# Optimization experiments

Measured on AMD Instinct MI355X. Metric: run time of the kernel, lower is better.

## Reference

```python
import jax, jax.numpy as jnp
import numpy as np

N_NODES = 100000
N_EDGES = 1600000
DIMS = [64, 64, 64, 32]  # [n_feat] + hid


def setup_inputs() -> dict:
    key = jax.random.key(0)
    ks = jax.random.split(key, 2 + 2 * (len(DIMS) - 1))
    x = jax.random.normal(ks[0], (N_NODES, DIMS[0]), dtype=jnp.float32)
    edge_index = jax.random.randint(ks[1], (2, N_EDGES), 0, N_NODES, dtype=jnp.int64)
    inp = {"x": x, "edge_index": edge_index}
    for i in range(len(DIMS) - 1):
        fan_in, fan_out = DIMS[i], DIMS[i + 1]
        scale = 1.0 / np.sqrt(fan_in)
        inp[f"W{i+1}"] = jax.random.normal(ks[2 + 2 * i], (fan_in, fan_out), dtype=jnp.float32) * scale
        inp[f"b{i+1}"] = jax.random.normal(ks[3 + 2 * i], (fan_out,), dtype=jnp.float32) * scale
    return inp


def _gcn_conv(x, W, b, src, dst, dis):
    # h = X W ; out[i] = sum_{j->i} norm_ij * h[j] + dis[i]^2 * h[i] + b
    h = x @ W
    norm = dis[src] * dis[dst]                      # [E]
    agg = jax.ops.segment_sum(h[src] * norm[:, None], dst, num_segments=x.shape[0])
    agg = agg + h * (dis * dis)[:, None]            # self-loop contribution
    return agg + b


def reference(x, edge_index, W1, b1, W2, b2, W3, b3):
    src, dst = edge_index[0], edge_index[1]
    n = x.shape[0]
    # degree with self-loops (edge weight 1), symmetric normalization
    deg = jax.ops.segment_sum(jnp.ones(src.shape[0], x.dtype), dst, num_segments=n) + 1.0
    dis = jax.lax.rsqrt(deg)
    h = jax.nn.relu(_gcn_conv(x, W1, b1, src, dst, dis))   # dropout is identity in eval
    h = jax.nn.relu(_gcn_conv(h, W2, b2, src, dst, dis))
    return _gcn_conv(h, W3, b3, src, dst, dis)
```

## Files before the change

### kernel.cpp

```cpp
#include <hip/hip_runtime.h>


typedef __attribute__((ext_vector_type(8))) _Float16 half8;

static inline int cdiv(int a, int b) { return (a + b - 1) / b; }

#define ACHUNK 8192
#define MAXNBK 512

__global__ void k_bucket_hist(const int* __restrict__ dst, int* __restrict__ counts_t,
                              int NBK, int NBA, int E) {
    __shared__ int cnt[MAXNBK];
    int t = threadIdx.x, b = blockIdx.x;
    for (int i = t; i < NBK; i += 256) cnt[i] = 0;
    __syncthreads();
    int e0 = b * ACHUNK;
#pragma unroll 8
    for (int j = 0; j < ACHUNK / 256; ++j) {
        int e = e0 + j * 256 + t;
        if (e < E) atomicAdd(&cnt[dst[e] >> 8], 1);
    }
    __syncthreads();
    for (int i = t; i < NBK; i += 256) counts_t[i * NBA + b] = cnt[i];
}

#define SCAN_T 256
#define SCAN_V 4
#define SCAN_CHUNK 1024

__global__ void k_scan_partial(const int* __restrict__ a, int* __restrict__ bsum, int n) {
    __shared__ int red[SCAN_T];
    int t = threadIdx.x, b = blockIdx.x;
    int base = b * SCAN_CHUNK + t * SCAN_V;
    int s = 0;
#pragma unroll
    for (int j = 0; j < SCAN_V; ++j) { int i = base + j; if (i < n) s += a[i]; }
    red[t] = s;
    __syncthreads();
    for (int off = SCAN_T / 2; off > 0; off >>= 1) {
        if (t < off) red[t] += red[t + off];
        __syncthreads();
    }
    if (t == 0) bsum[b] = red[0];
}

__global__ void k_scan_final(const int* __restrict__ a, const int* __restrict__ bsum,
                             int* __restrict__ out, int nb, int n) {
    __shared__ int sb[256];
    __shared__ int sh[SCAN_T];
    int t = threadIdx.x, bk = blockIdx.x;
    sb[t] = (t < nb) ? bsum[t] : 0;
    __syncthreads();
    for (int off = 1; off < 256; off <<= 1) {
        int u = (t >= off) ? sb[t - off] : 0;
        __syncthreads();
        sb[t] += u;
        __syncthreads();
    }
    int bbase = (bk == 0) ? 0 : sb[bk - 1];
    int base = bk * SCAN_CHUNK + t * SCAN_V;
    int v[SCAN_V];
    int s = 0;
#pragma unroll
    for (int j = 0; j < SCAN_V; ++j) {
        int i = base + j;
        v[j] = (i < n) ? a[i] : 0;
        s += v[j];
    }
    sh[t] = s;
    __syncthreads();
    for (int off = 1; off < SCAN_T; off <<= 1) {
        int u = (t >= off) ? sh[t - off] : 0;
        __syncthreads();
        sh[t] += u;
        __syncthreads();
    }
    int run = sh[t] - s + bbase;
#pragma unroll
    for (int j = 0; j < SCAN_V; ++j) {
        int i = base + j;
        if (i < n) { out[i] = run; run += v[j]; }
    }
}

__global__ void k_bucket_scatter(const int* __restrict__ src, const int* __restrict__ dst,
                                 const int* __restrict__ offsets, unsigned* __restrict__ bucketed,
                                 int NBK, int NBA, int E) {
    __shared__ int curs[MAXNBK];
    int t = threadIdx.x, b = blockIdx.x;
    for (int i = t; i < NBK; i += 256) curs[i] = offsets[i * NBA + b];
    __syncthreads();
    int e0 = b * ACHUNK;
#pragma unroll 8
    for (int j = 0; j < ACHUNK / 256; ++j) {
        int e = e0 + j * 256 + t;
        if (e < E) {
            int d = dst[e];
            int pos = atomicAdd(&curs[d >> 8], 1);
            bucketed[pos] = (unsigned)src[e] | ((unsigned)(d & 255) << 24);
        }
    }
}

__global__ void k_bucket_build(const unsigned* __restrict__ bucketed,
                               const int* __restrict__ offsets,
                               int* __restrict__ csr_src, int* __restrict__ row_start,
                               float* __restrict__ dis, int NBK, int NBA, int N, int E) {
    __shared__ int cnt[256];
    __shared__ int sc[256];
    int t = threadIdx.x, k = blockIdx.x;
    int base = offsets[k * NBA];
    int end = (k + 1 < NBK) ? offsets[(k + 1) * NBA] : E;
    cnt[t] = 0;
    __syncthreads();
    for (int i = base + t; i < end; i += 256)
        atomicAdd(&cnt[bucketed[i] >> 24], 1);
    __syncthreads();
    int c = cnt[t];
    sc[t] = c;
    __syncthreads();
    for (int off = 1; off < 256; off <<= 1) {
        int u = (t >= off) ? sc[t - off] : 0;
        __syncthreads();
        sc[t] += u;
        __syncthreads();
    }
    int excl = sc[t] - c;
    int node = k * 256 + t;
    if (node < N) {
        row_start[node] = base + excl;
        dis[node] = rsqrtf(1.0f + (float)c);
    }
    if (k == 0 && t == 0) row_start[N] = E;
    cnt[t] = base + excl;
    __syncthreads();
    for (int i = base + t; i < end; i += 256) {
        unsigned w = bucketed[i];
        int pos = atomicAdd(&cnt[w >> 24], 1);
        csr_src[pos] = (int)(w & 0xFFFFFFu);
    }
}

template <int K, int M>
__device__ inline void gemm_core(const float* Ws, const float* Xs,
                                 const float* __restrict__ dis,
                                 _Float16* __restrict__ H, int row0, int n) {
    constexpr int CPT = 8;
    constexpr int TPR = M / CPT;
    constexpr int KP = K + 1;
    int tid = threadIdx.x;
    int r = tid / TPR, c0 = (tid % TPR) * CPT;
    int row = row0 + r;
    if (row >= n) return;
    float4 a0 = make_float4(0.f, 0.f, 0.f, 0.f);
    float4 a1 = make_float4(0.f, 0.f, 0.f, 0.f);
#pragma unroll
    for (int k = 0; k < K; ++k) {
        float xv = Xs[r * KP + k];
        float4 w0 = ((const float4*)Ws)[(k * M + c0) / 4];
        float4 w1 = ((const float4*)Ws)[(k * M + c0) / 4 + 1];
        a0.x = fmaf(xv, w0.x, a0.x);
        a0.y = fmaf(xv, w0.y, a0.y);
        a0.z = fmaf(xv, w0.z, a0.z);
        a0.w = fmaf(xv, w0.w, a0.w);
        a1.x = fmaf(xv, w1.x, a1.x);
        a1.y = fmaf(xv, w1.y, a1.y);
        a1.z = fmaf(xv, w1.z, a1.z);
        a1.w = fmaf(xv, w1.w, a1.w);
    }
    float dn = dis[row];
    half8 hv;
    hv[0] = (_Float16)(a0.x * dn);
    hv[1] = (_Float16)(a0.y * dn);
    hv[2] = (_Float16)(a0.z * dn);
    hv[3] = (_Float16)(a0.w * dn);
    hv[4] = (_Float16)(a1.x * dn);
    hv[5] = (_Float16)(a1.y * dn);
    hv[6] = (_Float16)(a1.z * dn);
    hv[7] = (_Float16)(a1.w * dn);
    ((half8*)H)[(size_t)row * (M / CPT) + c0 / CPT] = hv;
}

template <int K, int M>
__global__ void k_gemm_f(const float* __restrict__ X, const float* __restrict__ W,
                         const float* __restrict__ dis, _Float16* __restrict__ H, int n) {
    constexpr int TPR = M / 8;
    constexpr int ROWS = 256 / TPR;
    constexpr int KP = K + 1;
    __shared__ float Ws[K * M];
    __shared__ float Xs[ROWS * KP];
    int tid = threadIdx.x;
    for (int idx = tid; idx < K * M / 4; idx += 256)
        ((float4*)Ws)[idx] = ((const float4*)W)[idx];
    int row0 = blockIdx.x * ROWS;
    for (int idx = tid; idx < ROWS * (K / 4); idx += 256) {
        int r = idx / (K / 4), kq = idx % (K / 4);
        int row = row0 + r;
        float4 vv = (row < n) ? ((const float4*)X)[(size_t)row * (K / 4) + kq]
                              : make_float4(0.f, 0.f, 0.f, 0.f);
        Xs[r * KP + kq * 4 + 0] = vv.x;
        Xs[r * KP + kq * 4 + 1] = vv.y;
        Xs[r * KP + kq * 4 + 2] = vv.z;
        Xs[r * KP + kq * 4 + 3] = vv.w;
    }
    __syncthreads();
    gemm_core<K, M>(Ws, Xs, dis, H, row0, n);
}

template <int K, int M>
__global__ void k_gemm_h(const _Float16* __restrict__ X, const float* __restrict__ W,
                         const float* __restrict__ dis, _Float16* __restrict__ H, int n) {
    constexpr int TPR = M / 8;
    constexpr int ROWS = 256 / TPR;
    constexpr int KP = K + 1;
    __shared__ float Ws[K * M];
    __shared__ float Xs[ROWS * KP];
    int tid = threadIdx.x;
    for (int idx = tid; idx < K * M / 4; idx += 256)
        ((float4*)Ws)[idx] = ((const float4*)W)[idx];
    int row0 = blockIdx.x * ROWS;
    for (int idx = tid; idx < ROWS * (K / 8); idx += 256) {
        int r = idx / (K / 8), kq = idx % (K / 8);
        int row = row0 + r;
        if (row < n) {
            half8 v = ((const half8*)X)[(size_t)row * (K / 8) + kq];
#pragma unroll
            for (int j = 0; j < 8; ++j) Xs[r * KP + kq * 8 + j] = (float)v[j];
        } else {
#pragma unroll
            for (int j = 0; j < 8; ++j) Xs[r * KP + kq * 8 + j] = 0.f;
        }
    }
    __syncthreads();
    gemm_core<K, M>(Ws, Xs, dis, H, row0, n);
}

__device__ inline void store8(float* out, int node, int fl, int LPN, const float* r) {
    float4* op = (float4*)(out + ((size_t)node * LPN + fl) * 8);
    op[0] = make_float4(r[0], r[1], r[2], r[3]);
    op[1] = make_float4(r[4], r[5], r[6], r[7]);
}
__device__ inline void store8(_Float16* out, int node, int fl, int LPN, const float* r) {
    half8 v;
#pragma unroll
    for (int j = 0; j < 8; ++j) v[j] = (_Float16)r[j];
    ((half8*)out)[(size_t)node * LPN + fl] = v;
}

template <int M, bool RELU, typename OutT>
__global__ void k_aggregate(const _Float16* __restrict__ h, const float* __restrict__ dis,
                            const int* __restrict__ row_start, const int* __restrict__ csr_src,
                            const float* __restrict__ b, OutT* __restrict__ out, int n) {
    constexpr int LPN = M / 8;
    constexpr int NPW = 64 / LPN;
    int gtid = blockIdx.x * blockDim.x + threadIdx.x;
    int wave = gtid >> 6;
    int lane = threadIdx.x & 63;
    int sub = lane / LPN, fl = lane % LPN;
    int node = wave * NPW + sub;
    if (node >= n) return;
    const half8* h8 = (const half8*)h;
    float acc[8];
#pragma unroll
    for (int j = 0; j < 8; ++j) acc[j] = 0.f;
    int e = row_start[node], e1 = row_start[node + 1];
    for (; e + 1 < e1; e += 2) {
        int s0 = csr_src[e];
        int s1 = csr_src[e + 1];
        half8 v0 = h8[(size_t)s0 * LPN + fl];
        half8 v1 = h8[(size_t)s1 * LPN + fl];
#pragma unroll
        for (int j = 0; j < 8; ++j) acc[j] += (float)v0[j] + (float)v1[j];
    }
    if (e < e1) {
        int s0 = csr_src[e];
        half8 v0 = h8[(size_t)s0 * LPN + fl];
#pragma unroll
        for (int j = 0; j < 8; ++j) acc[j] += (float)v0[j];
    }
    float dn = dis[node];
    half8 hv = h8[(size_t)node * LPN + fl];
    float4 b0 = ((const float4*)b)[fl * 2];
    float4 b1 = ((const float4*)b)[fl * 2 + 1];
    float r[8];
    r[0] = (acc[0] + (float)hv[0]) * dn + b0.x;
    r[1] = (acc[1] + (float)hv[1]) * dn + b0.y;
    r[2] = (acc[2] + (float)hv[2]) * dn + b0.z;
    r[3] = (acc[3] + (float)hv[3]) * dn + b0.w;
    r[4] = (acc[4] + (float)hv[4]) * dn + b1.x;
    r[5] = (acc[5] + (float)hv[5]) * dn + b1.y;
    r[6] = (acc[6] + (float)hv[6]) * dn + b1.z;
    r[7] = (acc[7] + (float)hv[7]) * dn + b1.w;
    if (RELU) {
#pragma unroll
        for (int j = 0; j < 8; ++j) r[j] = fmaxf(r[j], 0.f);
    }
    store8(out, node, fl, LPN, r);
}

extern "C" void kernel_launch(void* const* d_in, const int* in_sizes, int n_in,
                              void* d_out, int out_size, void* d_ws, size_t ws_size,
                              hipStream_t stream) {
    const float* x   = (const float*)d_in[0];
    const int*   ei  = (const int*)d_in[1];
    const float* W1  = (const float*)d_in[2];
    const float* b1  = (const float*)d_in[3];
    const float* W2  = (const float*)d_in[4];
    const float* b2  = (const float*)d_in[5];
    const float* W3  = (const float*)d_in[6];
    const float* b3  = (const float*)d_in[7];
    float* out = (float*)d_out;

    const int N = in_sizes[0] / 64;
    const int E = in_sizes[1] / 2;
    const int* src = ei;
    const int* dst = ei + E;

    const int NBK = cdiv(N, 256);
    const int NBA = cdiv(E, ACHUNK);
    const int nmat = NBK * NBA;

    const size_t Np = (size_t)((N + 63) / 64) * 64;
    char* p = (char*)d_ws;
    int*      counts_t = (int*)p;      p += (size_t)nmat * sizeof(int);
    int*      offsets  = (int*)p;      p += (size_t)nmat * sizeof(int);
    int*      bsum     = (int*)p;      p += 1024 * sizeof(int);
    int*      row_start= (int*)p;      p += (Np + 64) * sizeof(int);
    float*    dis      = (float*)p;    p += Np * sizeof(float);
    unsigned* bucketed = (unsigned*)p; p += (size_t)E * sizeof(unsigned);
    int*      csr_src  = (int*)p;      p += (size_t)E * sizeof(int);
    _Float16* bufH     = (_Float16*)p; p += Np * 64 * sizeof(_Float16);
    _Float16* bufX     = (_Float16*)p; p += Np * 64 * sizeof(_Float16);
    (void)ws_size;

    const int B = 256;
    const int nb = cdiv(nmat, SCAN_CHUNK);

    k_bucket_hist<<<NBA, B, 0, stream>>>(dst, counts_t, NBK, NBA, E);
    k_scan_partial<<<nb, B, 0, stream>>>(counts_t, bsum, nmat);
    k_scan_final<<<nb, B, 0, stream>>>(counts_t, bsum, offsets, nb, nmat);
    k_bucket_scatter<<<NBA, B, 0, stream>>>(src, dst, offsets, bucketed, NBK, NBA, E);
    k_bucket_build<<<NBK, B, 0, stream>>>(bucketed, offsets, csr_src, row_start, dis,
                                          NBK, NBA, N, E);

    const int blocks_a64 = cdiv(cdiv(N, 8) * 64, B);
    const int blocks_a32 = cdiv(cdiv(N, 16) * 64, B);

    k_gemm_f<64, 64><<<cdiv(N, 32), B, 0, stream>>>(x, W1, dis, bufH, N);
    k_aggregate<64, true, _Float16><<<blocks_a64, B, 0, stream>>>(
        bufH, dis, row_start, csr_src, b1, bufX, N);

    k_gemm_h<64, 64><<<cdiv(N, 32), B, 0, stream>>>(bufX, W2, dis, bufH, N);
    k_aggregate<64, true, _Float16><<<blocks_a64, B, 0, stream>>>(
        bufH, dis, row_start, csr_src, b2, bufX, N);

    k_gemm_h<64, 32><<<cdiv(N, 64), B, 0, stream>>>(bufX, W3, dis, bufH, N);
    k_aggregate<32, false, float><<<blocks_a32, B, 0, stream>>>(
        bufH, dis, row_start, csr_src, b3, out, N);
}
```

Before: 342.2 us.

## Fuse neighbor aggregation with next-layer GEMM and unroll edge loop by four

Replaces the separate aggregate and GEMM kernels for layers 1→2 and 2→3 with one kernel. Each block aggregates 32 nodes into shared memory, applies bias and ReLU, then multiplies by the next weight matrix. This removes the round trip of the intermediate fp16 activation through global memory and two kernel launches. The edge loop is also unrolled by four to keep more gathers in flight. In exchange, blocks are larger and use more shared memory. For the 32-wide output layer only half the threads do GEMM work.

```diff
diff --git a/kernel.cpp b/kernel.cpp
--- a/kernel.cpp
+++ b/kernel.cpp
@@ -139,46 +139,6 @@
         int pos = atomicAdd(&cnt[w >> 24], 1);
         csr_src[pos] = (int)(w & 0xFFFFFFu);
     }
-}
-
-template <int K, int M>
-__device__ inline void gemm_core(const float* Ws, const float* Xs,
-                                 const float* __restrict__ dis,
-                                 _Float16* __restrict__ H, int row0, int n) {
-    constexpr int CPT = 8;
-    constexpr int TPR = M / CPT;
-    constexpr int KP = K + 1;
-    int tid = threadIdx.x;
-    int r = tid / TPR, c0 = (tid % TPR) * CPT;
-    int row = row0 + r;
-    if (row >= n) return;
-    float4 a0 = make_float4(0.f, 0.f, 0.f, 0.f);
-    float4 a1 = make_float4(0.f, 0.f, 0.f, 0.f);
-#pragma unroll
-    for (int k = 0; k < K; ++k) {
-        float xv = Xs[r * KP + k];
-        float4 w0 = ((const float4*)Ws)[(k * M + c0) / 4];
-        float4 w1 = ((const float4*)Ws)[(k * M + c0) / 4 + 1];
-        a0.x = fmaf(xv, w0.x, a0.x);
-        a0.y = fmaf(xv, w0.y, a0.y);
-        a0.z = fmaf(xv, w0.z, a0.z);
-        a0.w = fmaf(xv, w0.w, a0.w);
-        a1.x = fmaf(xv, w1.x, a1.x);
-        a1.y = fmaf(xv, w1.y, a1.y);
-        a1.z = fmaf(xv, w1.z, a1.z);
-        a1.w = fmaf(xv, w1.w, a1.w);
-    }
-    float dn = dis[row];
-    half8 hv;
-    hv[0] = (_Float16)(a0.x * dn);
-    hv[1] = (_Float16)(a0.y * dn);
-    hv[2] = (_Float16)(a0.z * dn);
-    hv[3] = (_Float16)(a0.w * dn);
-    hv[4] = (_Float16)(a1.x * dn);
-    hv[5] = (_Float16)(a1.y * dn);
-    hv[6] = (_Float16)(a1.z * dn);
-    hv[7] = (_Float16)(a1.w * dn);
-    ((half8*)H)[(size_t)row * (M / CPT) + c0 / CPT] = hv;
 }
 
 template <int K, int M>
@@ -204,55 +164,131 @@
         Xs[r * KP + kq * 4 + 3] = vv.w;
     }
     __syncthreads();
-    gemm_core<K, M>(Ws, Xs, dis, H, row0, n);
-}
-
-template <int K, int M>
-__global__ void k_gemm_h(const _Float16* __restrict__ X, const float* __restrict__ W,
-                         const float* __restrict__ dis, _Float16* __restrict__ H, int n) {
-    constexpr int TPR = M / 8;
-    constexpr int ROWS = 256 / TPR;
-    constexpr int KP = K + 1;
-    __shared__ float Ws[K * M];
-    __shared__ float Xs[ROWS * KP];
+    int r = tid / TPR, c0 = (tid % TPR) * 8;
+    int row = row0 + r;
+    if (row >= n) return;
+    float4 a0 = make_float4(0.f, 0.f, 0.f, 0.f);
+    float4 a1 = make_float4(0.f, 0.f, 0.f, 0.f);
+#pragma unroll
+    for (int k = 0; k < K; ++k) {
+        float xv = Xs[r * KP + k];
+        float4 w0 = ((const float4*)Ws)[(k * M + c0) / 4];
+        float4 w1 = ((const float4*)Ws)[(k * M + c0) / 4 + 1];
+        a0.x = fmaf(xv, w0.x, a0.x);
+        a0.y = fmaf(xv, w0.y, a0.y);
+        a0.z = fmaf(xv, w0.z, a0.z);
+        a0.w = fmaf(xv, w0.w, a0.w);
+        a1.x = fmaf(xv, w1.x, a1.x);
+        a1.y = fmaf(xv, w1.y, a1.y);
+        a1.z = fmaf(xv, w1.z, a1.z);
+        a1.w = fmaf(xv, w1.w, a1.w);
+    }
+    float dn = dis[row];
+    half8 hv;
+    hv[0] = (_Float16)(a0.x * dn);
+    hv[1] = (_Float16)(a0.y * dn);
+    hv[2] = (_Float16)(a0.z * dn);
+    hv[3] = (_Float16)(a0.w * dn);
+    hv[4] = (_Float16)(a1.x * dn);
+    hv[5] = (_Float16)(a1.y * dn);
+    hv[6] = (_Float16)(a1.z * dn);
+    hv[7] = (_Float16)(a1.w * dn);
+    ((half8*)H)[(size_t)row * (M / 8) + c0 / 8] = hv;
+}
+
+template <int MOUT>
+__global__ void k_fused_agg_gemm(const _Float16* __restrict__ h, const float* __restrict__ dis,
+                                 const int* __restrict__ row_start, const int* __restrict__ csr_src,
+                                 const float* __restrict__ bagg, const float* __restrict__ W,
+                                 _Float16* __restrict__ H, int n) {
+    constexpr int K = 64, KP = K + 1;
+    __shared__ float Ws[K * MOUT];
+    __shared__ float Xs[32 * KP];
     int tid = threadIdx.x;
-    for (int idx = tid; idx < K * M / 4; idx += 256)
+    for (int idx = tid; idx < K * MOUT / 4; idx += 256)
         ((float4*)Ws)[idx] = ((const float4*)W)[idx];
-    int row0 = blockIdx.x * ROWS;
-    for (int idx = tid; idx < ROWS * (K / 8); idx += 256) {
-        int r = idx / (K / 8), kq = idx % (K / 8);
-        int row = row0 + r;
-        if (row < n) {
-            half8 v = ((const half8*)X)[(size_t)row * (K / 8) + kq];
-#pragma unroll
-            for (int j = 0; j < 8; ++j) Xs[r * KP + kq * 8 + j] = (float)v[j];
-        } else {
-#pragma unroll
-            for (int j = 0; j < 8; ++j) Xs[r * KP + kq * 8 + j] = 0.f;
+
+    int wave = tid >> 6, lane = tid & 63;
+    int sub = lane >> 3, fl = lane & 7;
+    int node0 = blockIdx.x * 32;
+    int node = node0 + wave * 8 + sub;
+    if (node < n) {
+        const half8* h8 = (const half8*)h;
+        float acc[8];
+#pragma unroll
+        for (int j = 0; j < 8; ++j) acc[j] = 0.f;
+        int e = row_start[node], e1 = row_start[node + 1];
+        for (; e + 3 < e1; e += 4) {
+            int s0 = csr_src[e], s1 = csr_src[e + 1];
+            int s2 = csr_src[e + 2], s3 = csr_src[e + 3];
+            half8 v0 = h8[(size_t)s0 * 8 + fl];
+            half8 v1 = h8[(size_t)s1 * 8 + fl];
+            half8 v2 = h8[(size_t)s2 * 8 + fl];
+            half8 v3 = h8[(size_t)s3 * 8 + fl];
+#pragma unroll
+            for (int j = 0; j < 8; ++j)
+                acc[j] += ((float)v0[j] + (float)v1[j]) + ((float)v2[j] + (float)v3[j]);
         }
-    }
-    __syncthreads();
-    gemm_core<K, M>(Ws, Xs, dis, H, row0, n);
-}
-
-__device__ inline void store8(float* out, int node, int fl, int LPN, const float* r) {
-    float4* op = (float4*)(out + ((size_t)node * LPN + fl) * 8);
-    op[0] = make_float4(r[0], r[1], r[2], r[3]);
-    op[1] = make_float4(r[4], r[5], r[6], r[7]);
-}
-__device__ inline void store8(_Float16* out, int node, int fl, int LPN, const float* r) {
-    half8 v;
-#pragma unroll
-    for (int j = 0; j < 8; ++j) v[j] = (_Float16)r[j];
-    ((half8*)out)[(size_t)node * LPN + fl] = v;
-}
-
-template <int M, bool RELU, typename OutT>
-__global__ void k_aggregate(const _Float16* __restrict__ h, const float* __restrict__ dis,
-                            const int* __restrict__ row_start, const int* __restrict__ csr_src,
-                            const float* __restrict__ b, OutT* __restrict__ out, int n) {
-    constexpr int LPN = M / 8;
-    constexpr int NPW = 64 / LPN;
+        for (; e < e1; ++e) {
+            int s0 = csr_src[e];
+            half8 v0 = h8[(size_t)s0 * 8 + fl];
+#pragma unroll
+            for (int j = 0; j < 8; ++j) acc[j] += (float)v0[j];
+        }
+        float dn = dis[node];
+        half8 hv = h8[(size_t)node * 8 + fl];
+        float4 b0 = ((const float4*)bagg)[fl * 2];
+        float4 b1 = ((const float4*)bagg)[fl * 2 + 1];
+        int rrow = wave * 8 + sub;
+        float* xp = &Xs[rrow * KP + fl * 8];
+        xp[0] = fmaxf((acc[0] + (float)hv[0]) * dn + b0.x, 0.f);
+        xp[1] = fmaxf((acc[1] + (float)hv[1]) * dn + b0.y, 0.f);
+        xp[2] = fmaxf((acc[2] + (float)hv[2]) * dn + b0.z, 0.f);
+        xp[3] = fmaxf((acc[3] + (float)hv[3]) * dn + b0.w, 0.f);
+        xp[4] = fmaxf((acc[4] + (float)hv[4]) * dn + b1.x, 0.f);
+        xp[5] = fmaxf((acc[5] + (float)hv[5]) * dn + b1.y, 0.f);
+        xp[6] = fmaxf((acc[6] + (float)hv[6]) * dn + b1.z, 0.f);
+        xp[7] = fmaxf((acc[7] + (float)hv[7]) * dn + b1.w, 0.f);
+    }
+    __syncthreads();
+
+    constexpr int TPR = MOUT / 8;
+    int r = tid / TPR, c0 = (tid % TPR) * 8;
+    int row = node0 + r;
+    if (r >= 32 || row >= n) return;
+    float4 a0 = make_float4(0.f, 0.f, 0.f, 0.f);
+    float4 a1 = make_float4(0.f, 0.f, 0.f, 0.f);
+#pragma unroll
+    for (int k = 0; k < K; ++k) {
+        float xv = Xs[r * KP + k];
+        float4 w0 = ((const float4*)Ws)[(k * MOUT + c0) / 4];
+        float4 w1 = ((const float4*)Ws)[(k * MOUT + c0) / 4 + 1];
+        a0.x = fmaf(xv, w0.x, a0.x);
+        a0.y = fmaf(xv, w0.y, a0.y);
+        a0.z = fmaf(xv, w0.z, a0.z);
+        a0.w = fmaf(xv, w0.w, a0.w);
+        a1.x = fmaf(xv, w1.x, a1.x);
+        a1.y = fmaf(xv, w1.y, a1.y);
+        a1.z = fmaf(xv, w1.z, a1.z);
+        a1.w = fmaf(xv, w1.w, a1.w);
+    }
+    float dn = dis[row];
+    half8 hv;
+    hv[0] = (_Float16)(a0.x * dn);
+    hv[1] = (_Float16)(a0.y * dn);
+    hv[2] = (_Float16)(a0.z * dn);
+    hv[3] = (_Float16)(a0.w * dn);
+    hv[4] = (_Float16)(a1.x * dn);
+    hv[5] = (_Float16)(a1.y * dn);
+    hv[6] = (_Float16)(a1.z * dn);
+    hv[7] = (_Float16)(a1.w * dn);
+    ((half8*)H)[(size_t)row * (MOUT / 8) + c0 / 8] = hv;
+}
+
+__global__ void k_aggregate32(const _Float16* __restrict__ h, const float* __restrict__ dis,
+                              const int* __restrict__ row_start, const int* __restrict__ csr_src,
+                              const float* __restrict__ b, float* __restrict__ out, int n) {
+    constexpr int LPN = 4, NPW = 16;
     int gtid = blockIdx.x * blockDim.x + threadIdx.x;
     int wave = gtid >> 6;
     int lane = threadIdx.x & 63;
@@ -264,15 +300,18 @@
 #pragma unroll
     for (int j = 0; j < 8; ++j) acc[j] = 0.f;
     int e = row_start[node], e1 = row_start[node + 1];
-    for (; e + 1 < e1; e += 2) {
-        int s0 = csr_src[e];
-        int s1 = csr_src[e + 1];
+    for (; e + 3 < e1; e += 4) {
+        int s0 = csr_src[e], s1 = csr_src[e + 1];
+        int s2 = csr_src[e + 2], s3 = csr_src[e + 3];
         half8 v0 = h8[(size_t)s0 * LPN + fl];
         half8 v1 = h8[(size_t)s1 * LPN + fl];
-#pragma unroll
-        for (int j = 0; j < 8; ++j) acc[j] += (float)v0[j] + (float)v1[j];
-    }
-    if (e < e1) {
+        half8 v2 = h8[(size_t)s2 * LPN + fl];
+        half8 v3 = h8[(size_t)s3 * LPN + fl];
+#pragma unroll
+        for (int j = 0; j < 8; ++j)
+            acc[j] += ((float)v0[j] + (float)v1[j]) + ((float)v2[j] + (float)v3[j]);
+    }
+    for (; e < e1; ++e) {
         int s0 = csr_src[e];
         half8 v0 = h8[(size_t)s0 * LPN + fl];
 #pragma unroll
@@ -282,20 +321,15 @@
     half8 hv = h8[(size_t)node * LPN + fl];
     float4 b0 = ((const float4*)b)[fl * 2];
     float4 b1 = ((const float4*)b)[fl * 2 + 1];
-    float r[8];
-    r[0] = (acc[0] + (float)hv[0]) * dn + b0.x;
-    r[1] = (acc[1] + (float)hv[1]) * dn + b0.y;
-    r[2] = (acc[2] + (float)hv[2]) * dn + b0.z;
-    r[3] = (acc[3] + (float)hv[3]) * dn + b0.w;
-    r[4] = (acc[4] + (float)hv[4]) * dn + b1.x;
-    r[5] = (acc[5] + (float)hv[5]) * dn + b1.y;
-    r[6] = (acc[6] + (float)hv[6]) * dn + b1.z;
-    r[7] = (acc[7] + (float)hv[7]) * dn + b1.w;
-    if (RELU) {
-#pragma unroll
-        for (int j = 0; j < 8; ++j) r[j] = fmaxf(r[j], 0.f);
-    }
-    store8(out, node, fl, LPN, r);
+    float4* op = (float4*)(out + ((size_t)node * LPN + fl) * 8);
+    op[0] = make_float4((acc[0] + (float)hv[0]) * dn + b0.x,
+                        (acc[1] + (float)hv[1]) * dn + b0.y,
+                        (acc[2] + (float)hv[2]) * dn + b0.z,
+                        (acc[3] + (float)hv[3]) * dn + b0.w);
+    op[1] = make_float4((acc[4] + (float)hv[4]) * dn + b1.x,
+                        (acc[5] + (float)hv[5]) * dn + b1.y,
+                        (acc[6] + (float)hv[6]) * dn + b1.z,
+                        (acc[7] + (float)hv[7]) * dn + b1.w);
 }
 
 extern "C" void kernel_launch(void* const* d_in, const int* in_sizes, int n_in,
@@ -329,8 +363,8 @@
     float*    dis      = (float*)p;    p += Np * sizeof(float);
     unsigned* bucketed = (unsigned*)p; p += (size_t)E * sizeof(unsigned);
     int*      csr_src  = (int*)p;      p += (size_t)E * sizeof(int);
-    _Float16* bufH     = (_Float16*)p; p += Np * 64 * sizeof(_Float16);
-    _Float16* bufX     = (_Float16*)p; p += Np * 64 * sizeof(_Float16);
+    _Float16* bufA     = (_Float16*)p; p += Np * 64 * sizeof(_Float16);
+    _Float16* bufB     = (_Float16*)p; p += Np * 64 * sizeof(_Float16);
     (void)ws_size;
 
     const int B = 256;
@@ -343,18 +377,11 @@
     k_bucket_build<<<NBK, B, 0, stream>>>(bucketed, offsets, csr_src, row_start, dis,
                                           NBK, NBA, N, E);
 
-    const int blocks_a64 = cdiv(cdiv(N, 8) * 64, B);
-    const int blocks_a32 = cdiv(cdiv(N, 16) * 64, B);
-
-    k_gemm_f<64, 64><<<cdiv(N, 32), B, 0, stream>>>(x, W1, dis, bufH, N);
-    k_aggregate<64, true, _Float16><<<blocks_a64, B, 0, stream>>>(
-        bufH, dis, row_start, csr_src, b1, bufX, N);
-
-    k_gemm_h<64, 64><<<cdiv(N, 32), B, 0, stream>>>(bufX, W2, dis, bufH, N);
-    k_aggregate<64, true, _Float16><<<blocks_a64, B, 0, stream>>>(
-        bufH, dis, row_start, csr_src, b2, bufX, N);
-
-    k_gemm_h<64, 32><<<cdiv(N, 64), B, 0, stream>>>(bufX, W3, dis, bufH, N);
-    k_aggregate<32, false, float><<<blocks_a32, B, 0, stream>>>(
-        bufH, dis, row_start, csr_src, b3, out, N);
-}
+    k_gemm_f<64, 64><<<cdiv(N, 32), B, 0, stream>>>(x, W1, dis, bufA, N);
+    k_fused_agg_gemm<64><<<cdiv(N, 32), B, 0, stream>>>(
+        bufA, dis, row_start, csr_src, b1, W2, bufB, N);
+    k_fused_agg_gemm<32><<<cdiv(N, 32), B, 0, stream>>>(
+        bufB, dis, row_start, csr_src, b2, W3, bufA, N);
+    k_aggregate32<<<cdiv(cdiv(N, 16) * 64, B), B, 0, stream>>>(
+        bufA, dis, row_start, csr_src, b3, out, N);
+}
```

Result: faster. 299.3 us (-12.5%).
